# Kernel optimization log

Measured on AMD Instinct MI355X. Metric: run time of the kernel, lower is better.

The kernel has to match this reference:

```python
import jax, jax.numpy as jnp
import numpy as np

MAXV = 127.0  # 2**(8-1) - 1, signed int8


def setup_inputs() -> dict:
    key = jax.random.key(0)
    k1, k2, k3 = jax.random.split(key, 3)
    N, K, M = 8192, 4096, 4096  # tokens, size_in, size_out
    x = jax.random.normal(k1, (N, K), dtype=jnp.float32)
    weight = jax.random.normal(k2, (M, K), dtype=jnp.float32) * 0.02
    bias = jax.random.normal(k3, (M,), dtype=jnp.float32) * 0.01
    amax_x = jnp.array([3.0], dtype=jnp.float32)   # calibrated activation amax
    amax_w = jnp.array([0.06], dtype=jnp.float32)  # calibrated weight amax
    return {"x": x, "weight": weight, "bias": bias, "amax_x": amax_x, "amax_w": amax_w}


def _quantize_int8(v, amax):
    # TensorQuantizer with fake_quant=False: scale to int grid, round, clamp to [-127, 127]
    return jnp.clip(jnp.round(v * (MAXV / amax)), -MAXV, MAXV).astype(jnp.int8)


def reference(x, weight, bias, amax_x, amax_w):
    qx = _quantize_int8(x, amax_x)          # [N, K] int8
    qw = _quantize_int8(weight, amax_w)     # [M, K] int8
    acc = jnp.matmul(qx.astype(jnp.int32), qw.T.astype(jnp.int32))  # [N, M] int32
    scale = (MAXV / amax_x) * (MAXV / amax_w)  # combined dequant scale
    out = acc.astype(jnp.float32) / scale
    return out + bias
```

## Files before the change

### kernel.cpp

```cpp
#include <hip/hip_runtime.h>

typedef __attribute__((ext_vector_type(4))) int i32x4;

__device__ __forceinline__ void gload_lds16(const void* g, void* l) {
  __builtin_amdgcn_global_load_lds((const __attribute__((address_space(1))) void*)g,
                                   (__attribute__((address_space(3))) void*)l,
                                   16, 0, 0);
}

__device__ __forceinline__ int swz4(int r) { return (r ^ (r >> 2)) & 3; }

__global__ void quant_i8_kernel(const float* __restrict__ in,
                                signed char* __restrict__ out,
                                const float* __restrict__ amax, int n4) {
  const float s = 127.0f / amax[0];
  int i = blockIdx.x * blockDim.x + threadIdx.x;
  const int stride = gridDim.x * blockDim.x;
  const float4* __restrict__ in4 = (const float4*)in;
  int* __restrict__ o4 = (int*)out;
  for (; i < n4; i += stride) {
    float4 v = in4[i];
    int q0 = (int)rintf(fminf(fmaxf(v.x * s, -127.0f), 127.0f));
    int q1 = (int)rintf(fminf(fmaxf(v.y * s, -127.0f), 127.0f));
    int q2 = (int)rintf(fminf(fmaxf(v.z * s, -127.0f), 127.0f));
    int q3 = (int)rintf(fminf(fmaxf(v.w * s, -127.0f), 127.0f));
    o4[i] = (q0 & 255) | ((q1 & 255) << 8) | ((q2 & 255) << 16) | ((q3 & 255) << 24);
  }
}

__global__ __launch_bounds__(256, 2) void gemm_i8_kernel(
    const signed char* __restrict__ qx,
    const signed char* __restrict__ qw,
    const float* __restrict__ bias,
    const float* __restrict__ amax_x,
    const float* __restrict__ amax_w,
    float* __restrict__ out,
    int N, int M, int K) {
  constexpr int BM = 128;
  constexpr int BN = 128;
  constexpr int BK = 64;

  __shared__ alignas(16) signed char As[BM * BK];
  __shared__ alignas(16) signed char Bs[BN * BK];

  const int tid  = threadIdx.x;
  const int wid  = tid >> 6;
  const int lane = tid & 63;
  const int l15  = lane & 15;
  const int l4   = lane >> 4;

  const int rowBase = blockIdx.y * BM;
  const int colBase = blockIdx.x * BN;

  const int wRow = (wid >> 1) * 64;
  const int wCol = (wid & 1) * 64;

  const int tr = tid >> 2;
  const int tp = tid & 3;
  const int ra = tr, rb = tr + 64;
  const int ca0 = (tp ^ swz4(ra)) * 16;
  const int ca1 = (tp ^ swz4(rb)) * 16;

  const signed char* srcA0 = qx + (size_t)(rowBase + ra) * K + ca0;
  const signed char* srcA1 = qx + (size_t)(rowBase + rb) * K + ca1;
  const signed char* srcB0 = qw + (size_t)(colBase + ra) * K + ca0;
  const signed char* srcB1 = qw + (size_t)(colBase + rb) * K + ca1;

  i32x4 acc[4][4] = {};

  int offA[4], offB[4];
#pragma unroll
  for (int i = 0; i < 4; ++i) {
    int r = wRow + i * 16 + l15;
    offA[i] = r * 64 + (l4 ^ swz4(r)) * 16;
    int c = wCol + i * 16 + l15;
    offB[i] = c * 64 + (l4 ^ swz4(c)) * 16;
  }

  for (int kt = 0; kt < K; kt += BK) {
    gload_lds16(srcA0 + kt, As + tid * 16);
    gload_lds16(srcA1 + kt, As + 4096 + tid * 16);
    gload_lds16(srcB0 + kt, Bs + tid * 16);
    gload_lds16(srcB1 + kt, Bs + 4096 + tid * 16);
    __syncthreads();

    i32x4 a[4], b[4];
#pragma unroll
    for (int i = 0; i < 4; ++i) a[i] = *(const i32x4*)(As + offA[i]);
#pragma unroll
    for (int j = 0; j < 4; ++j) b[j] = *(const i32x4*)(Bs + offB[j]);

#pragma unroll
    for (int i = 0; i < 4; ++i)
#pragma unroll
      for (int j = 0; j < 4; ++j)
        acc[i][j] = __builtin_amdgcn_mfma_i32_16x16x64_i8(a[i], b[j], acc[i][j], 0, 0, 0);

    __syncthreads();
  }

  const float dq = amax_x[0] * amax_w[0] * (1.0f / (127.0f * 127.0f));
#pragma unroll
  for (int j = 0; j < 4; ++j) {
    const int col = colBase + wCol + j * 16 + l15;
    const float bv = bias[col];
#pragma unroll
    for (int i = 0; i < 4; ++i) {
      const int row = rowBase + wRow + i * 16 + l4 * 4;
#pragma unroll
      for (int r = 0; r < 4; ++r) {
        out[(size_t)(row + r) * M + col] = (float)acc[i][j][r] * dq + bv;
      }
    }
  }
}

extern "C" void kernel_launch(void* const* d_in, const int* in_sizes, int n_in,
                              void* d_out, int out_size, void* d_ws, size_t ws_size,
                              hipStream_t stream) {
  const float* x      = (const float*)d_in[0];
  const float* w      = (const float*)d_in[1];
  const float* bias   = (const float*)d_in[2];
  const float* amax_x = (const float*)d_in[3];
  const float* amax_w = (const float*)d_in[4];
  float* out = (float*)d_out;

  const int M = in_sizes[2];
  const int K = in_sizes[1] / M;
  const int N = (int)((long)in_sizes[0] / K);

  signed char* qx = (signed char*)d_ws;
  signed char* qw = qx + (size_t)N * K;

  quant_i8_kernel<<<2048, 256, 0, stream>>>(x, qx, amax_x, N * (K / 4));
  quant_i8_kernel<<<2048, 256, 0, stream>>>(w, qw, amax_w, M * (K / 4));

  dim3 grid(M / 128, N / 128);
  gemm_i8_kernel<<<grid, 256, 0, stream>>>(qx, qw, bias, amax_x, amax_w, out,
                                           N, M, K);
}
```

Baseline: 220.4 us.

## Rewrite int8 GEMM with 256x128 tiles, double-buffered LDS, XCD swizzle, fused quant

Replaces the GEMM with a 512-thread 256x128 tile kernel that double-buffers LDS and issues the next stage's global-to-LDS loads before the MFMAs, using manual waitcnt and barriers. It remaps workgroups with an XCD-aware swizzle, changes the LDS bank swizzle, and raises MFMA priority. The two quantize launches are merged into one kernel. The aim is to hide global load latency and cut launch overhead, at the cost of higher register use from the larger accumulator tile and fragile hand-written synchronisation.

```diff
diff --git a/kernel.cpp b/kernel.cpp
--- a/kernel.cpp
+++ b/kernel.cpp
@@ -8,27 +8,38 @@
                                    16, 0, 0);
 }
 
-__device__ __forceinline__ int swz4(int r) { return (r ^ (r >> 2)) & 3; }
+#define BARRIER() __builtin_amdgcn_s_barrier()
+#define LGKM0()   asm volatile("s_waitcnt lgkmcnt(0)" ::: "memory")
+#define VMCNT3()  asm volatile("s_waitcnt vmcnt(3)" ::: "memory")
 
-__global__ void quant_i8_kernel(const float* __restrict__ in,
-                                signed char* __restrict__ out,
-                                const float* __restrict__ amax, int n4) {
-  const float s = 127.0f / amax[0];
+__global__ void quant_both_kernel(const float* __restrict__ x,
+                                  const float* __restrict__ w,
+                                  signed char* __restrict__ qx,
+                                  signed char* __restrict__ qw,
+                                  const float* __restrict__ amax_x,
+                                  const float* __restrict__ amax_w,
+                                  int nx4, int nw4) {
+  const float sx = 127.0f / amax_x[0];
+  const float sw = 127.0f / amax_w[0];
   int i = blockIdx.x * blockDim.x + threadIdx.x;
   const int stride = gridDim.x * blockDim.x;
-  const float4* __restrict__ in4 = (const float4*)in;
-  int* __restrict__ o4 = (int*)out;
-  for (; i < n4; i += stride) {
-    float4 v = in4[i];
+  const int ntot = nx4 + nw4;
+  for (; i < ntot; i += stride) {
+    const bool isx = i < nx4;
+    const float4* src = isx ? (const float4*)x : (const float4*)w;
+    int* dst = isx ? (int*)qx : (int*)qw;
+    const int j = isx ? i : i - nx4;
+    const float s = isx ? sx : sw;
+    float4 v = src[j];
     int q0 = (int)rintf(fminf(fmaxf(v.x * s, -127.0f), 127.0f));
     int q1 = (int)rintf(fminf(fmaxf(v.y * s, -127.0f), 127.0f));
     int q2 = (int)rintf(fminf(fmaxf(v.z * s, -127.0f), 127.0f));
     int q3 = (int)rintf(fminf(fmaxf(v.w * s, -127.0f), 127.0f));
-    o4[i] = (q0 & 255) | ((q1 & 255) << 8) | ((q2 & 255) << 16) | ((q3 & 255) << 24);
+    dst[j] = (q0 & 255) | ((q1 & 255) << 8) | ((q2 & 255) << 16) | ((q3 & 255) << 24);
   }
 }
 
-__global__ __launch_bounds__(256, 2) void gemm_i8_kernel(
+__global__ __launch_bounds__(512, 4) void gemm_i8_bk64(
     const signed char* __restrict__ qx,
     const signed char* __restrict__ qw,
     const float* __restrict__ bias,
@@ -36,83 +47,111 @@
     const float* __restrict__ amax_w,
     float* __restrict__ out,
     int N, int M, int K) {
-  constexpr int BM = 128;
-  constexpr int BN = 128;
-  constexpr int BK = 64;
+  constexpr int BKB = 64;
 
-  __shared__ alignas(16) signed char As[BM * BK];
-  __shared__ alignas(16) signed char Bs[BN * BK];
+  __shared__ signed char lds[49152];
 
   const int tid  = threadIdx.x;
+  const int lane = tid & 63;
   const int wid  = tid >> 6;
-  const int lane = tid & 63;
+  const int wm   = wid >> 2;
+  const int wn   = wid & 3;
   const int l15  = lane & 15;
   const int l4   = lane >> 4;
 
-  const int rowBase = blockIdx.y * BM;
-  const int colBase = blockIdx.x * BN;
+  const int nbn = M >> 7;
+  const int nwg = (N >> 8) * nbn;
+  const int cpx = nwg >> 3;
+  const int swz = (blockIdx.x & 7) * cpx + (blockIdx.x >> 3);
+  const int rowBase = (swz / nbn) << 8;
+  const int colBase = (swz % nbn) << 7;
 
-  const int wRow = (wid >> 1) * 64;
-  const int wCol = (wid & 1) * 64;
+  const signed char* srcA[2];
+#pragma unroll
+  for (int L = 0; L < 2; ++L) {
+    const int slot = L * 512 + tid;
+    const int row  = slot >> 2;
+    const int c    = (slot & 3) ^ ((row >> 1) & 3);
+    srcA[L] = qx + (size_t)(rowBase + row) * K + c * 16;
+  }
+  const int rowB = tid >> 2;
+  const int cB   = (tid & 3) ^ ((rowB >> 1) & 3);
+  const signed char* srcB = qw + (size_t)(colBase + rowB) * K + cB * 16;
 
-  const int tr = tid >> 2;
-  const int tp = tid & 3;
-  const int ra = tr, rb = tr + 64;
-  const int ca0 = (tp ^ swz4(ra)) * 16;
-  const int ca1 = (tp ^ swz4(rb)) * 16;
+  signed char* A[2] = {lds, lds + 16384};
+  signed char* B[2] = {lds + 32768, lds + 40960};
 
-  const signed char* srcA0 = qx + (size_t)(rowBase + ra) * K + ca0;
-  const signed char* srcA1 = qx + (size_t)(rowBase + rb) * K + ca1;
-  const signed char* srcB0 = qw + (size_t)(colBase + ra) * K + ca0;
-  const signed char* srcB1 = qw + (size_t)(colBase + rb) * K + ca1;
+#define STAGE(p, kt)                                                   \
+  do {                                                                 \
+    gload_lds16(srcA[0] + (kt) * BKB, A[p] + tid * 16);                \
+    gload_lds16(srcA[1] + (kt) * BKB, A[p] + 8192 + tid * 16);         \
+    gload_lds16(srcB + (kt) * BKB, B[p] + tid * 16);                   \
+  } while (0)
 
-  i32x4 acc[4][4] = {};
+  i32x4 acc[8][2] = {{{0}}};
+  i32x4 af[8];
+  i32x4 bf[2];
 
-  int offA[4], offB[4];
+  int offA[8], offB[2];
 #pragma unroll
-  for (int i = 0; i < 4; ++i) {
-    int r = wRow + i * 16 + l15;
-    offA[i] = r * 64 + (l4 ^ swz4(r)) * 16;
-    int c = wCol + i * 16 + l15;
-    offB[i] = c * 64 + (l4 ^ swz4(c)) * 16;
+  for (int mi = 0; mi < 8; ++mi) {
+    const int r = wm * 128 + mi * 16 + l15;
+    offA[mi] = r * 64 + ((l4 ^ ((r >> 1) & 3)) * 16);
+  }
+#pragma unroll
+  for (int nj = 0; nj < 2; ++nj) {
+    const int r = wn * 32 + nj * 16 + l15;
+    offB[nj] = r * 64 + ((l4 ^ ((r >> 1) & 3)) * 16);
   }
 
-  for (int kt = 0; kt < K; kt += BK) {
-    gload_lds16(srcA0 + kt, As + tid * 16);
-    gload_lds16(srcA1 + kt, As + 4096 + tid * 16);
-    gload_lds16(srcB0 + kt, Bs + tid * 16);
-    gload_lds16(srcB1 + kt, Bs + 4096 + tid * 16);
-    __syncthreads();
+#define PHASE(p, ktStage)                                                     \
+  do {                                                                        \
+    _Pragma("unroll") for (int mi = 0; mi < 8; ++mi)                          \
+        af[mi] = *(const i32x4*)(A[p] + offA[mi]);                            \
+    _Pragma("unroll") for (int nj = 0; nj < 2; ++nj)                          \
+        bf[nj] = *(const i32x4*)(B[p] + offB[nj]);                            \
+    LGKM0();                                                                  \
+    BARRIER();                          \
+    STAGE(p, ktStage);                                                        \
+    __builtin_amdgcn_s_setprio(1);                                            \
+    _Pragma("unroll") for (int mi = 0; mi < 8; ++mi)                          \
+        _Pragma("unroll") for (int nj = 0; nj < 2; ++nj)                      \
+            acc[mi][nj] = __builtin_amdgcn_mfma_i32_16x16x64_i8(              \
+                af[mi], bf[nj], acc[mi][nj], 0, 0, 0);                        \
+    __builtin_amdgcn_s_setprio(0);                                            \
+    VMCNT3();             \
+    BARRIER();                                          \
+  } while (0)
 
-    i32x4 a[4], b[4];
-#pragma unroll
-    for (int i = 0; i < 4; ++i) a[i] = *(const i32x4*)(As + offA[i]);
-#pragma unroll
-    for (int j = 0; j < 4; ++j) b[j] = *(const i32x4*)(Bs + offB[j]);
+  const int T = K / BKB;
 
-#pragma unroll
-    for (int i = 0; i < 4; ++i)
-#pragma unroll
-      for (int j = 0; j < 4; ++j)
-        acc[i][j] = __builtin_amdgcn_mfma_i32_16x16x64_i8(a[i], b[j], acc[i][j], 0, 0, 0);
+  STAGE(0, 0);
+  STAGE(1, 1);
+  VMCNT3();
+  BARRIER();
 
-    __syncthreads();
+  for (int it = 0; it < T / 2; ++it) {
+    const int k2 = (2 * it + 2 < T) ? 2 * it + 2 : T - 1;
+    const int k3 = (2 * it + 3 < T) ? 2 * it + 3 : T - 1;
+    PHASE(0, k2);
+    PHASE(1, k3);
   }
 
   const float dq = amax_x[0] * amax_w[0] * (1.0f / (127.0f * 127.0f));
 #pragma unroll
-  for (int j = 0; j < 4; ++j) {
-    const int col = colBase + wCol + j * 16 + l15;
+  for (int nj = 0; nj < 2; ++nj) {
+    const int col = colBase + wn * 32 + nj * 16 + l15;
     const float bv = bias[col];
 #pragma unroll
-    for (int i = 0; i < 4; ++i) {
-      const int row = rowBase + wRow + i * 16 + l4 * 4;
+    for (int mi = 0; mi < 8; ++mi) {
+      const int row = rowBase + wm * 128 + mi * 16 + l4 * 4;
 #pragma unroll
-      for (int r = 0; r < 4; ++r) {
-        out[(size_t)(row + r) * M + col] = (float)acc[i][j][r] * dq + bv;
-      }
+      for (int r = 0; r < 4; ++r)
+        out[(size_t)(row + r) * M + col] = (float)acc[mi][nj][r] * dq + bv;
     }
   }
+#undef STAGE
+#undef PHASE
 }
 
 extern "C" void kernel_launch(void* const* d_in, const int* in_sizes, int n_in,
@@ -132,10 +171,12 @@
   signed char* qx = (signed char*)d_ws;
   signed char* qw = qx + (size_t)N * K;
 
-  quant_i8_kernel<<<2048, 256, 0, stream>>>(x, qx, amax_x, N * (K / 4));
-  quant_i8_kernel<<<2048, 256, 0, stream>>>(w, qw, amax_w, M * (K / 4));
+  const int nx4 = N * (K / 4);
+  const int nw4 = M * (K / 4);
+  quant_both_kernel<<<2048, 256, 0, stream>>>(x, w, qx, qw, amax_x, amax_w,
+                                              nx4, nw4);
 
-  dim3 grid(M / 128, N / 128);
-  gemm_i8_kernel<<<grid, 256, 0, stream>>>(qx, qw, bias, amax_x, amax_w, out,
-                                           N, M, K);
+  const int nwg = (N / 256) * (M / 128);
+  gemm_i8_bk64<<<nwg, 512, 0, stream>>>(qx, qw, bias, amax_x, amax_w, out,
+                                        N, M, K);
 }
```

Measured after the change: 217.4 us. Within noise of the previous version (-1.4%).
